# Kernel optimization log

Hardware: AMD Instinct MI355X
Metric: run time of the kernel (lower is better)

Reference implementation:

```python
import jax, jax.numpy as jnp
import numpy as np

K = 3  # kernel_size
STRIDE, PAD, DIL = 1, 1, 1


def conv2d(x, w, b):
    out = jax.lax.conv_general_dilated(
        x, w, (STRIDE, STRIDE), [(PAD, PAD), (PAD, PAD)],
        rhs_dilation=(DIL, DIL), dimension_numbers=('NCHW', 'OIHW', 'NCHW'))
    return out + b[None, :, None, None]


def bilinear_sample(x, sy, sx):
    """grid_sample(mode=bilinear, padding_mode=zeros, align_corners=True).
    x: (B,C,H,W); sy,sx: (B,K2,Ho,Wo) pixel coords. Returns (B,C,K2,Ho,Wo)."""
    B, C, H, W = x.shape
    y0 = jnp.floor(sy); x0 = jnp.floor(sx)
    y1 = y0 + 1.0;      x1 = x0 + 1.0
    wy1 = sy - y0; wy0 = 1.0 - wy1
    wx1 = sx - x0; wx0 = 1.0 - wx1
    x_flat = x.reshape(B, C, H * W)

    def gather(iy, ix):
        mask = ((iy >= 0) & (iy <= H - 1) & (ix >= 0) & (ix <= W - 1)).astype(x.dtype)
        iyc = jnp.clip(iy, 0, H - 1).astype(jnp.int32)
        ixc = jnp.clip(ix, 0, W - 1).astype(jnp.int32)
        idx = (iyc * W + ixc).reshape(B, 1, -1)
        v = jnp.take_along_axis(x_flat, idx, axis=2).reshape(B, C, *iy.shape[1:])
        return v * mask[:, None]

    return (gather(y0, x0) * (wy0 * wx0)[:, None]
            + gather(y0, x1) * (wy0 * wx1)[:, None]
            + gather(y1, x0) * (wy1 * wx0)[:, None]
            + gather(y1, x1) * (wy1 * wx1)[:, None])


def setup_inputs() -> dict:
    key = jax.random.key(0)
    ks = jax.random.split(key, 6)
    B, C, H, W = 4, 64, 128, 128
    O = 64
    x = jax.random.normal(ks[0], (B, C, H, W), jnp.float32)
    weight = jax.random.normal(ks[1], (O, C, K, K), jnp.float32) * (1.0 / (C * K * K) ** 0.5)
    bias = jax.random.normal(ks[2], (O,), jnp.float32) * 0.1
    offset_w = jax.random.normal(ks[3], (2 * K * K, C, K, K), jnp.float32) * 0.1 / (C * K * K) ** 0.5
    offset_b = jnp.zeros((2 * K * K,), jnp.float32)
    mod_w = jax.random.normal(ks[4], (K * K, C, K, K), jnp.float32) * (1.0 / (C * K * K) ** 0.5)
    mod_b = jnp.ones((K * K,), jnp.float32)
    return {"x": x, "weight": weight, "bias": bias,
            "offset_w": offset_w, "offset_b": offset_b,
            "mod_w": mod_w, "mod_b": mod_b}


def reference(x, weight, bias, offset_w, offset_b, mod_w, mod_b):
    B, C, H, W = x.shape
    O = weight.shape[0]
    K2 = K * K
    Ho = (H + 2 * PAD - DIL * (K - 1) - 1) // STRIDE + 1
    Wo = (W + 2 * PAD - DIL * (K - 1) - 1) // STRIDE + 1

    offsets = conv2d(x, offset_w, offset_b)                # (B, 2*K2, Ho, Wo)
    modul = jax.nn.sigmoid(conv2d(x, mod_w, mod_b))        # (B, K2, Ho, Wo)

    off = offsets.reshape(B, 2, K2, Ho, Wo)
    off_y, off_x = off[:, 0], off[:, 1]

    base_y, base_x = jnp.meshgrid(jnp.arange(Ho, dtype=jnp.float32),
                                  jnp.arange(Wo, dtype=jnp.float32), indexing='ij')
    base_y = base_y * STRIDE - PAD + (K // 2) * DIL
    base_x = base_x * STRIDE - PAD + (K // 2) * DIL
    koffs = jnp.arange(-(K // 2), K // 2 + 1, dtype=jnp.float32)
    ky, kx = jnp.meshgrid(koffs, koffs, indexing='ij')
    ky = ky.reshape(-1); kx = kx.reshape(-1)               # (K2,)

    sample_y = base_y[None, None] + ky[None, :, None, None] + off_y  # (B,K2,Ho,Wo)
    sample_x = base_x[None, None] + kx[None, :, None, None] + off_x
    # torch code normalizes to [-1,1] with align_corners=True; pixel coords are
    # recovered identically, so we sample directly at (sample_y, sample_x).

    sampled = bilinear_sample(x, sample_y, sample_x)       # (B,C,K2,Ho,Wo)

    w_flat = weight.reshape(O, C, K2)
    out = jnp.einsum('bckhw,ock->bohw', sampled, w_flat)   # groups=1

    mod_mean = jnp.mean(modul, axis=1, keepdims=True)      # (B,1,Ho,Wo)
    out = out * mod_mean + bias[None, :, None, None]
    return out
```

## Files before the change

### kernel.cpp

```cpp
#include <hip/hip_runtime.h>
#include <math.h>

#define K 3
#define K2 9
#define BB 4
#define C 64
#define H 128
#define W 128
#define O 64
#define HW (H*W)
#define Ho 128
#define Wo 128
#define TILE 64
#define TSTR 80

typedef _Float16 half4v __attribute__((ext_vector_type(4)));
typedef _Float16 half8v __attribute__((ext_vector_type(8)));
typedef float float4v __attribute__((ext_vector_type(4)));

__device__ __forceinline__ half8v bcast8(_Float16 w) {
    half8v v = {w, w, w, w, w, w, w, w};
    return v;
}

__global__ __launch_bounds__(256) void prep_all(
    const float* __restrict__ x,
    const float* __restrict__ weight,
    const float* __restrict__ offset_w,
    const float* __restrict__ mod_w,
    _Float16* __restrict__ xh,
    _Float16* __restrict__ wB,
    _Float16* __restrict__ wAB)
{
    int t = threadIdx.x;
    if (blockIdx.x < BB * H) {
        __shared__ _Float16 tile[W][68];
        int by = blockIdx.x;
        int y = by % H, b = by / H;
        int xq = t & 31, cr = t >> 5;
        #pragma unroll
        for (int g = 0; g < 8; g++) {
            int c = g * 8 + cr;
            float4v v = *(const float4v*)&x[(((size_t)b * C + c) * H + y) * W + xq * 4];
            tile[xq * 4 + 0][c] = (_Float16)v[0];
            tile[xq * 4 + 1][c] = (_Float16)v[1];
            tile[xq * 4 + 2][c] = (_Float16)v[2];
            tile[xq * 4 + 3][c] = (_Float16)v[3];
        }
        __syncthreads();
        int xp2 = t >> 1, hf = t & 1;
        const _Float16* src = &tile[xp2][hf * 32];
        _Float16* dst = xh + (((size_t)b * H + y) * W + xp2) * 64 + hf * 32;
        #pragma unroll
        for (int i = 0; i < 8; i++)
            *(half4v*)(dst + i * 4) = *(const half4v*)(src + i * 4);
    } else {
        int i = (blockIdx.x - BB * H) * 256 + t;
        if (i < K2 * 2 * 4 * 64 * 8) {
            int jj = i & 7;
            int lane = (i >> 3) & 63;
            int q4 = (i >> 9) & 3;
            int i2 = i >> 11;
            int tap = i2 >> 1, s = i2 & 1;
            int ch = s * 32 + ((lane >> 4) & 3) * 8 + jj;
            int o = q4 * 16 + (lane & 15);
            wB[i] = (_Float16)weight[(o * C + ch) * 9 + tap];
        }
        if (i < K2 * 2 * 2 * 64 * 8) {
            int jj = i & 7;
            int lane = (i >> 3) & 63;
            int jt = (i >> 9) & 1;
            int i2 = i >> 10;
            int tap = i2 >> 1, s = i2 & 1;
            int ch = s * 32 + ((lane >> 4) & 3) * 8 + jj;
            int n = jt * 16 + (lane & 15);
            float wv = 0.f;
            if (n < 27)
                wv = (n < 18) ? offset_w[(n * C + ch) * 9 + tap]
                              : mod_w[((n - 18) * C + ch) * 9 + tap];
            wAB[i] = (_Float16)wv;
        }
    }
}

__global__ __launch_bounds__(256) void fused_kernel(
    const _Float16* __restrict__ xh,
    const _Float16* __restrict__ wB,
    const _Float16* __restrict__ wAB,
    const float* __restrict__ bias,
    const float* __restrict__ offset_b,
    const float* __restrict__ mod_b,
    float* __restrict__ out)
{
    __shared__ _Float16 s_T[2][TILE][TSTR];
    __shared__ unsigned int s_ai[K2 * TILE];
    __shared__ half4v s_wgt[K2 * TILE];
    __shared__ float s_mm[TILE];
    float* s_res = (float*)&s_T[0][0][0];
    float* s_out = (float*)&s_T[0][0][0];

    int blk = blockIdx.x;
    int xcd = blk & 7, idx = blk >> 3;
    int b  = xcd >> 1;
    int h  = ((xcd & 1) << 6) | (idx >> 1);
    int wt = idx & 1;
    int t  = threadIdx.x;
    int q  = t >> 6;
    int lane = t & 63;
    int m16 = lane & 15;
    int quad = (lane >> 4) & 3;
    int w0 = wt * TILE;
    int px = lane;
    int gpx0 = q * 16 + (lane >> 3);
    int seg  = lane & 7;

    const _Float16* xb = xh + (size_t)b * HW * 64;

    float4v acc2[2];
    #pragma unroll
    for (int jt = 0; jt < 2; jt++) { float4v z = {0.f,0.f,0.f,0.f}; acc2[jt] = z; }

    #pragma unroll
    for (int pg = 0; pg < 2; pg++) {
        int ppx = gpx0 + pg * 8;
        int y = h - 1;
        int xv = w0 + ppx - 1;
        float m = ((y >= 0) ? 1.f : 0.f) * ((xv >= 0) ? 1.f : 0.f);
        int yc = max(y, 0), xc = max(xv, 0);
        const _Float16* src = xb + ((size_t)(yc * W + xc)) * 64 + seg * 8;
        half8v v = *(const half8v*)src;
        *(half8v*)&s_T[0][ppx][seg * 8] = v * bcast8((_Float16)m);
    }
    __syncthreads();

    #pragma unroll 1
    for (int tap = 0; tap < K2; tap++) {
        half8v pv[2]; _Float16 pm[2];
        if (tap < 8) {
            int tp = tap + 1;
            int ki = tp / 3, kj = tp % 3;
            int y = h + ki - 1;
            float my = (y >= 0 && y < H) ? 1.f : 0.f;
            int yc = min(max(y, 0), H - 1);
            #pragma unroll
            for (int pg = 0; pg < 2; pg++) {
                int ppx = gpx0 + pg * 8;
                int xv = w0 + ppx + kj - 1;
                pm[pg] = (_Float16)(my * ((xv >= 0 && xv < W) ? 1.f : 0.f));
                int xc = min(max(xv, 0), W - 1);
                pv[pg] = *(const half8v*)(xb + ((size_t)(yc * W + xc)) * 64 + seg * 8);
            }
        }
        int row = q * 16 + m16;
        #pragma unroll
        for (int s = 0; s < 2; s++) {
            half8v af = *(const half8v*)&s_T[tap & 1][row][s * 32 + quad * 8];
            #pragma unroll
            for (int jt = 0; jt < 2; jt++) {
                int widx = (((tap * 2 + s) * 2 + jt) * 64 + lane) * 8;
                half8v bf = *(const half8v*)(wAB + widx);
                acc2[jt] = __builtin_amdgcn_mfma_f32_16x16x32_f16(af, bf, acc2[jt], 0, 0, 0);
            }
        }
        if (tap < 8) {
            #pragma unroll
            for (int pg = 0; pg < 2; pg++)
                *(half8v*)&s_T[(tap + 1) & 1][gpx0 + pg * 8][seg * 8] = pv[pg] * bcast8(pm[pg]);
        }
        __syncthreads();
    }

    #pragma unroll
    for (int jt = 0; jt < 2; jt++) {
        int n = jt * 16 + m16;
        if (n < 27) {
            #pragma unroll
            for (int r = 0; r < 4; r++)
                s_res[n * 65 + q * 16 + quad * 4 + r] = acc2[jt][r];
        }
    }
    __syncthreads();

    #pragma unroll
    for (int ee = 0; ee < 3; ee++) {
        int e = t + ee * 256;
        if (e < K2 * TILE) {
            int k = e >> 6, p = e & 63;
            float offy = s_res[k * 65 + p] + offset_b[k];
            float offx = s_res[(9 + k) * 65 + p] + offset_b[9 + k];
            float sy = (float)(h + k / 3 - 1) + offy;
            float sx = (float)(w0 + p + k % 3 - 1) + offx;
            float fy = floorf(sy), fx = floorf(sx);
            int y0 = (int)fy, x0 = (int)fx;
            float wy1 = sy - fy, wx1 = sx - fx;
            int y0c = min(max(y0, 0), H - 1), y1c = min(max(y0 + 1, 0), H - 1);
            int x0c = min(max(x0, 0), W - 1), x1c = min(max(x0 + 1, 0), W - 1);
            s_ai[e] = (unsigned int)(y0c * W + x0c)
                    | ((unsigned int)(x1c - x0c) << 14)
                    | ((unsigned int)(y1c - y0c) << 15);
            float wg0 = (1.f - wy1) * ((y0 >= 0 && y0 < H) ? 1.f : 0.f);
            float wg1 = wy1 * ((y0 + 1 >= 0 && y0 + 1 < H) ? 1.f : 0.f);
            float wg2 = (1.f - wx1) * ((x0 >= 0 && x0 < W) ? 1.f : 0.f);
            float wg3 = wx1 * ((x0 + 1 >= 0 && x0 + 1 < W) ? 1.f : 0.f);
            half4v wp4;
            wp4[0] = (_Float16)(wg0 * wg2);
            wp4[1] = (_Float16)(wg0 * wg3);
            wp4[2] = (_Float16)(wg1 * wg2);
            wp4[3] = (_Float16)(wg1 * wg3);
            s_wgt[e] = wp4;
        }
    }
    if (t < TILE) {
        float sm = 0.f;
        #pragma unroll
        for (int m = 0; m < 9; m++) {
            float z = s_res[(18 + m) * 65 + t] + mod_b[m];
            sm += 1.f / (1.f + expf(-z));
        }
        s_mm[t] = sm * (1.f / 9.f);
    }
    __syncthreads();

    float4v acc[4];
    #pragma unroll
    for (int i = 0; i < 4; i++) { float4v z = {0.f,0.f,0.f,0.f}; acc[i] = z; }

    #pragma unroll
    for (int pg = 0; pg < 2; pg++) {
        int ppx = gpx0 + pg * 8;
        unsigned int ai = s_ai[ppx];
        half4v wg = s_wgt[ppx];
        int a00 = ai & 0x3FFF;
        int dxo = ((ai >> 14) & 1) * 64;
        int dyo = ((ai >> 15) & 1) * (W * 64);
        const _Float16* base = xb + (size_t)a00 * 64 + seg * 8;
        half8v r00 = *(const half8v*)(base);
        half8v r01 = *(const half8v*)(base + dxo);
        half8v r10 = *(const half8v*)(base + dyo);
        half8v r11 = *(const half8v*)(base + dyo + dxo);
        half8v v = r00 * bcast8(wg[0]) + r01 * bcast8(wg[1])
                 + r10 * bcast8(wg[2]) + r11 * bcast8(wg[3]);
        *(half8v*)&s_T[0][ppx][seg * 8] = v;
    }
    __syncthreads();

    #pragma unroll 1
    for (int tap = 0; tap < K2; tap++) {
        half8v rr[2][4]; half4v wgp[2];
        if (tap < 8) {
            #pragma unroll
            for (int pg = 0; pg < 2; pg++) {
                int e = (tap + 1) * 64 + gpx0 + pg * 8;
                unsigned int ai = s_ai[e];
                wgp[pg] = s_wgt[e];
                int a00 = ai & 0x3FFF;
                int dxo = ((ai >> 14) & 1) * 64;
                int dyo = ((ai >> 15) & 1) * (W * 64);
                const _Float16* base = xb + (size_t)a00 * 64 + seg * 8;
                rr[pg][0] = *(const half8v*)(base);
                rr[pg][1] = *(const half8v*)(base + dxo);
                rr[pg][2] = *(const half8v*)(base + dyo);
                rr[pg][3] = *(const half8v*)(base + dyo + dxo);
            }
        }
        #pragma unroll
        for (int s = 0; s < 2; s++) {
            int widx = (((tap * 2 + s) * 4 + q) * 64 + lane) * 8;
            half8v bf = *(const half8v*)(wB + widx);
            #pragma unroll
            for (int i = 0; i < 4; i++) {
                half8v af = *(const half8v*)&s_T[tap & 1][i * 16 + m16][s * 32 + quad * 8];
                acc[i] = __builtin_amdgcn_mfma_f32_16x16x32_f16(af, bf, acc[i], 0, 0, 0);
            }
        }
        if (tap < 8) {
            #pragma unroll
            for (int pg = 0; pg < 2; pg++) {
                half4v wg = wgp[pg];
                half8v v = rr[pg][0] * bcast8(wg[0]) + rr[pg][1] * bcast8(wg[1])
                         + rr[pg][2] * bcast8(wg[2]) + rr[pg][3] * bcast8(wg[3]);
                *(half8v*)&s_T[(tap + 1) & 1][gpx0 + pg * 8][seg * 8] = v;
            }
        }
        __syncthreads();
    }

    #pragma unroll
    for (int i = 0; i < 4; i++) {
        int o = q * 16 + m16;
        #pragma unroll
        for (int r = 0; r < 4; r++)
            s_out[o * 65 + i * 16 + quad * 4 + r] = acc[i][r];
    }
    __syncthreads();
    {
        float mm = s_mm[px];
        #pragma unroll
        for (int jj = 0; jj < 16; jj++) {
            int o = q * 16 + jj;
            out[(((size_t)b * O + o) * Ho + h) * Wo + w0 + px] =
                s_out[o * 65 + px] * mm + bias[o];
        }
    }
}

extern "C" void kernel_launch(void* const* d_in, const int* in_sizes, int n_in,
                              void* d_out, int out_size, void* d_ws, size_t ws_size,
                              hipStream_t stream) {
    const float* x        = (const float*)d_in[0];
    const float* weight   = (const float*)d_in[1];
    const float* bias     = (const float*)d_in[2];
    const float* offset_w = (const float*)d_in[3];
    const float* offset_b = (const float*)d_in[4];
    const float* mod_w    = (const float*)d_in[5];
    const float* mod_b    = (const float*)d_in[6];
    float* out = (float*)d_out;

    _Float16* wB  = (_Float16*)d_ws;
    _Float16* wAB = wB + 36864;
    _Float16* xh  = wAB + 18432;

    prep_all<<<BB * H + 144, 256, 0, stream>>>(
        x, weight, offset_w, mod_w, xh, wB, wAB);

    int nblk = BB * Ho * (Wo / TILE);
    fused_kernel<<<nblk, 256, 0, stream>>>(
        xh, wB, wAB, bias, offset_b, mod_b, out);
}
```

Baseline: 109.4 us.

## Give each wave a private LDS pixel tile to drop per-tap block barriers

Splits the shared double-buffered tile so each wave owns its own 16 pixels. Each wave stages, for all 64 channels, the pixels it then feeds to MFMA, which removes the __syncthreads inside both tap loops. In the main conv, each wave now computes all 64 output channels for its 16 pixels instead of 16 channels for all 64 pixels. That means four weight fragments are loaded from global per k-step instead of one. The exchange is fewer block barriers against more global weight traffic and more registers. Intra-wave LDS ordering now depends only on wave-level execution.

```diff
diff --git a/kernel.cpp b/kernel.cpp
--- a/kernel.cpp
+++ b/kernel.cpp
@@ -92,12 +92,12 @@
     const float* __restrict__ mod_b,
     float* __restrict__ out)
 {
-    __shared__ _Float16 s_T[2][TILE][TSTR];
+    __shared__ _Float16 s_W[4][2][16][TSTR];
     __shared__ unsigned int s_ai[K2 * TILE];
     __shared__ half4v s_wgt[K2 * TILE];
     __shared__ float s_mm[TILE];
-    float* s_res = (float*)&s_T[0][0][0];
-    float* s_out = (float*)&s_T[0][0][0];
+    float* s_res = (float*)&s_W[0][0][0][0];
+    float* s_out = (float*)&s_W[0][0][0][0];
 
     int blk = blockIdx.x;
     int xcd = blk & 7, idx = blk >> 3;
@@ -111,8 +111,8 @@
     int quad = (lane >> 4) & 3;
     int w0 = wt * TILE;
     int px = lane;
-    int gpx0 = q * 16 + (lane >> 3);
-    int seg  = lane & 7;
+    int p4 = lane >> 2;
+    int sg = lane & 3;
 
     const _Float16* xb = xh + (size_t)b * HW * 64;
 
@@ -120,41 +120,35 @@
     #pragma unroll
     for (int jt = 0; jt < 2; jt++) { float4v z = {0.f,0.f,0.f,0.f}; acc2[jt] = z; }
 
-    #pragma unroll
-    for (int pg = 0; pg < 2; pg++) {
-        int ppx = gpx0 + pg * 8;
+    {
         int y = h - 1;
-        int xv = w0 + ppx - 1;
+        int xv = w0 + q * 16 + p4 - 1;
         float m = ((y >= 0) ? 1.f : 0.f) * ((xv >= 0) ? 1.f : 0.f);
         int yc = max(y, 0), xc = max(xv, 0);
-        const _Float16* src = xb + ((size_t)(yc * W + xc)) * 64 + seg * 8;
-        half8v v = *(const half8v*)src;
-        *(half8v*)&s_T[0][ppx][seg * 8] = v * bcast8((_Float16)m);
-    }
-    __syncthreads();
+        const _Float16* src = xb + ((size_t)(yc * W + xc)) * 64 + sg * 8;
+        half8v vm = bcast8((_Float16)m);
+        *(half8v*)&s_W[q][0][p4][sg * 8]      = *(const half8v*)src * vm;
+        *(half8v*)&s_W[q][0][p4][32 + sg * 8] = *(const half8v*)(src + 32) * vm;
+    }
 
     #pragma unroll 1
     for (int tap = 0; tap < K2; tap++) {
-        half8v pv[2]; _Float16 pm[2];
+        half8v n0, n1; _Float16 nm;
         if (tap < 8) {
             int tp = tap + 1;
             int ki = tp / 3, kj = tp % 3;
             int y = h + ki - 1;
-            float my = (y >= 0 && y < H) ? 1.f : 0.f;
-            int yc = min(max(y, 0), H - 1);
-            #pragma unroll
-            for (int pg = 0; pg < 2; pg++) {
-                int ppx = gpx0 + pg * 8;
-                int xv = w0 + ppx + kj - 1;
-                pm[pg] = (_Float16)(my * ((xv >= 0 && xv < W) ? 1.f : 0.f));
-                int xc = min(max(xv, 0), W - 1);
-                pv[pg] = *(const half8v*)(xb + ((size_t)(yc * W + xc)) * 64 + seg * 8);
-            }
-        }
-        int row = q * 16 + m16;
+            int xv = w0 + q * 16 + p4 + kj - 1;
+            nm = (_Float16)(((y >= 0 && y < H) ? 1.f : 0.f) *
+                            ((xv >= 0 && xv < W) ? 1.f : 0.f));
+            int yc = min(max(y, 0), H - 1), xc = min(max(xv, 0), W - 1);
+            const _Float16* src = xb + ((size_t)(yc * W + xc)) * 64 + sg * 8;
+            n0 = *(const half8v*)src;
+            n1 = *(const half8v*)(src + 32);
+        }
         #pragma unroll
         for (int s = 0; s < 2; s++) {
-            half8v af = *(const half8v*)&s_T[tap & 1][row][s * 32 + quad * 8];
+            half8v af = *(const half8v*)&s_W[q][tap & 1][m16][s * 32 + quad * 8];
             #pragma unroll
             for (int jt = 0; jt < 2; jt++) {
                 int widx = (((tap * 2 + s) * 2 + jt) * 64 + lane) * 8;
@@ -163,13 +157,13 @@
             }
         }
         if (tap < 8) {
-            #pragma unroll
-            for (int pg = 0; pg < 2; pg++)
-                *(half8v*)&s_T[(tap + 1) & 1][gpx0 + pg * 8][seg * 8] = pv[pg] * bcast8(pm[pg]);
-        }
-        __syncthreads();
-    }
-
+            half8v vm = bcast8(nm);
+            *(half8v*)&s_W[q][(tap + 1) & 1][p4][sg * 8]      = n0 * vm;
+            *(half8v*)&s_W[q][(tap + 1) & 1][p4][32 + sg * 8] = n1 * vm;
+        }
+    }
+
+    __syncthreads();
     #pragma unroll
     for (int jt = 0; jt < 2; jt++) {
         int n = jt * 16 + m16;
@@ -225,72 +219,72 @@
     #pragma unroll
     for (int i = 0; i < 4; i++) { float4v z = {0.f,0.f,0.f,0.f}; acc[i] = z; }
 
-    #pragma unroll
-    for (int pg = 0; pg < 2; pg++) {
-        int ppx = gpx0 + pg * 8;
-        unsigned int ai = s_ai[ppx];
-        half4v wg = s_wgt[ppx];
+    {
+        int e = q * 16 + p4;
+        unsigned int ai = s_ai[e];
+        half4v wg = s_wgt[e];
         int a00 = ai & 0x3FFF;
         int dxo = ((ai >> 14) & 1) * 64;
         int dyo = ((ai >> 15) & 1) * (W * 64);
-        const _Float16* base = xb + (size_t)a00 * 64 + seg * 8;
-        half8v r00 = *(const half8v*)(base);
-        half8v r01 = *(const half8v*)(base + dxo);
-        half8v r10 = *(const half8v*)(base + dyo);
-        half8v r11 = *(const half8v*)(base + dyo + dxo);
-        half8v v = r00 * bcast8(wg[0]) + r01 * bcast8(wg[1])
-                 + r10 * bcast8(wg[2]) + r11 * bcast8(wg[3]);
-        *(half8v*)&s_T[0][ppx][seg * 8] = v;
-    }
-    __syncthreads();
+        const _Float16* base = xb + (size_t)a00 * 64 + sg * 8;
+        half8v v0 = *(const half8v*)(base)             * bcast8(wg[0])
+                  + *(const half8v*)(base + dxo)       * bcast8(wg[1])
+                  + *(const half8v*)(base + dyo)       * bcast8(wg[2])
+                  + *(const half8v*)(base + dyo + dxo) * bcast8(wg[3]);
+        half8v v1 = *(const half8v*)(base + 32)             * bcast8(wg[0])
+                  + *(const half8v*)(base + 32 + dxo)       * bcast8(wg[1])
+                  + *(const half8v*)(base + 32 + dyo)       * bcast8(wg[2])
+                  + *(const half8v*)(base + 32 + dyo + dxo) * bcast8(wg[3]);
+        *(half8v*)&s_W[q][0][p4][sg * 8]      = v0;
+        *(half8v*)&s_W[q][0][p4][32 + sg * 8] = v1;
+    }
 
     #pragma unroll 1
     for (int tap = 0; tap < K2; tap++) {
-        half8v rr[2][4]; half4v wgp[2];
+        half8v rr[8]; half4v wgp;
         if (tap < 8) {
+            int e = (tap + 1) * 64 + q * 16 + p4;
+            unsigned int ai = s_ai[e];
+            wgp = s_wgt[e];
+            int a00 = ai & 0x3FFF;
+            int dxo = ((ai >> 14) & 1) * 64;
+            int dyo = ((ai >> 15) & 1) * (W * 64);
+            const _Float16* base = xb + (size_t)a00 * 64 + sg * 8;
+            rr[0] = *(const half8v*)(base);
+            rr[1] = *(const half8v*)(base + dxo);
+            rr[2] = *(const half8v*)(base + dyo);
+            rr[3] = *(const half8v*)(base + dyo + dxo);
+            rr[4] = *(const half8v*)(base + 32);
+            rr[5] = *(const half8v*)(base + 32 + dxo);
+            rr[6] = *(const half8v*)(base + 32 + dyo);
+            rr[7] = *(const half8v*)(base + 32 + dyo + dxo);
+        }
+        #pragma unroll
+        for (int s = 0; s < 2; s++) {
+            half8v af = *(const half8v*)&s_W[q][tap & 1][m16][s * 32 + quad * 8];
             #pragma unroll
-            for (int pg = 0; pg < 2; pg++) {
-                int e = (tap + 1) * 64 + gpx0 + pg * 8;
-                unsigned int ai = s_ai[e];
-                wgp[pg] = s_wgt[e];
-                int a00 = ai & 0x3FFF;
-                int dxo = ((ai >> 14) & 1) * 64;
-                int dyo = ((ai >> 15) & 1) * (W * 64);
-                const _Float16* base = xb + (size_t)a00 * 64 + seg * 8;
-                rr[pg][0] = *(const half8v*)(base);
-                rr[pg][1] = *(const half8v*)(base + dxo);
-                rr[pg][2] = *(const half8v*)(base + dyo);
-                rr[pg][3] = *(const half8v*)(base + dyo + dxo);
+            for (int ot = 0; ot < 4; ot++) {
+                int widx = (((tap * 2 + s) * 4 + ot) * 64 + lane) * 8;
+                half8v bf = *(const half8v*)(wB + widx);
+                acc[ot] = __builtin_amdgcn_mfma_f32_16x16x32_f16(af, bf, acc[ot], 0, 0, 0);
             }
         }
-        #pragma unroll
-        for (int s = 0; s < 2; s++) {
-            int widx = (((tap * 2 + s) * 4 + q) * 64 + lane) * 8;
-            half8v bf = *(const half8v*)(wB + widx);
-            #pragma unroll
-            for (int i = 0; i < 4; i++) {
-                half8v af = *(const half8v*)&s_T[tap & 1][i * 16 + m16][s * 32 + quad * 8];
-                acc[i] = __builtin_amdgcn_mfma_f32_16x16x32_f16(af, bf, acc[i], 0, 0, 0);
-            }
-        }
         if (tap < 8) {
-            #pragma unroll
-            for (int pg = 0; pg < 2; pg++) {
-                half4v wg = wgp[pg];
-                half8v v = rr[pg][0] * bcast8(wg[0]) + rr[pg][1] * bcast8(wg[1])
-                         + rr[pg][2] * bcast8(wg[2]) + rr[pg][3] * bcast8(wg[3]);
-                *(half8v*)&s_T[(tap + 1) & 1][gpx0 + pg * 8][seg * 8] = v;
-            }
-        }
-        __syncthreads();
-    }
-
-    #pragma unroll
-    for (int i = 0; i < 4; i++) {
-        int o = q * 16 + m16;
+            half8v v0 = rr[0] * bcast8(wgp[0]) + rr[1] * bcast8(wgp[1])
+                      + rr[2] * bcast8(wgp[2]) + rr[3] * bcast8(wgp[3]);
+            half8v v1 = rr[4] * bcast8(wgp[0]) + rr[5] * bcast8(wgp[1])
+                      + rr[6] * bcast8(wgp[2]) + rr[7] * bcast8(wgp[3]);
+            *(half8v*)&s_W[q][(tap + 1) & 1][p4][sg * 8]      = v0;
+            *(half8v*)&s_W[q][(tap + 1) & 1][p4][32 + sg * 8] = v1;
+        }
+    }
+
+    __syncthreads();
+    #pragma unroll
+    for (int ot = 0; ot < 4; ot++) {
         #pragma unroll
         for (int r = 0; r < 4; r++)
-            s_out[o * 65 + i * 16 + quad * 4 + r] = acc[i][r];
+            s_out[(ot * 16 + m16) * 65 + q * 16 + quad * 4 + r] = acc[ot][r];
     }
     __syncthreads();
     {
```

New measurement: 114.0 us. 4.2% more time.

## Load offset-conv input fragments directly from global, drop LDS staging and barriers

Applied to the files above, without the earlier changes.

The offset/modulation conv stage no longer stages each tap's input row through a double-buffered LDS tile with a barrier per tap. Each lane now loads its MFMA operand straight from global (L2-cached NHWC fp16) and swaps the A/B roles so pixels sit on the B side, which changes how results are written to s_res. The loop is also unrolled by 3. This removes nine __syncthreads and the LDS round trips, at the cost of more uncoalesced global loads and exposed load latency.

```diff
diff --git a/kernel.cpp b/kernel.cpp
--- a/kernel.cpp
+++ b/kernel.cpp
@@ -111,6 +111,8 @@
     int quad = (lane >> 4) & 3;
     int w0 = wt * TILE;
     int px = lane;
+    int pxg = q * 16 + m16;
+    int chq = quad * 8;
     int gpx0 = q * 16 + (lane >> 3);
     int seg  = lane & 7;
 
@@ -120,63 +122,32 @@
     #pragma unroll
     for (int jt = 0; jt < 2; jt++) { float4v z = {0.f,0.f,0.f,0.f}; acc2[jt] = z; }
 
-    #pragma unroll
-    for (int pg = 0; pg < 2; pg++) {
-        int ppx = gpx0 + pg * 8;
-        int y = h - 1;
-        int xv = w0 + ppx - 1;
-        float m = ((y >= 0) ? 1.f : 0.f) * ((xv >= 0) ? 1.f : 0.f);
-        int yc = max(y, 0), xc = max(xv, 0);
-        const _Float16* src = xb + ((size_t)(yc * W + xc)) * 64 + seg * 8;
-        half8v v = *(const half8v*)src;
-        *(half8v*)&s_T[0][ppx][seg * 8] = v * bcast8((_Float16)m);
-    }
-    __syncthreads();
-
-    #pragma unroll 1
+    #pragma unroll 3
     for (int tap = 0; tap < K2; tap++) {
-        half8v pv[2]; _Float16 pm[2];
-        if (tap < 8) {
-            int tp = tap + 1;
-            int ki = tp / 3, kj = tp % 3;
-            int y = h + ki - 1;
-            float my = (y >= 0 && y < H) ? 1.f : 0.f;
-            int yc = min(max(y, 0), H - 1);
-            #pragma unroll
-            for (int pg = 0; pg < 2; pg++) {
-                int ppx = gpx0 + pg * 8;
-                int xv = w0 + ppx + kj - 1;
-                pm[pg] = (_Float16)(my * ((xv >= 0 && xv < W) ? 1.f : 0.f));
-                int xc = min(max(xv, 0), W - 1);
-                pv[pg] = *(const half8v*)(xb + ((size_t)(yc * W + xc)) * 64 + seg * 8);
-            }
-        }
-        int row = q * 16 + m16;
-        #pragma unroll
-        for (int s = 0; s < 2; s++) {
-            half8v af = *(const half8v*)&s_T[tap & 1][row][s * 32 + quad * 8];
-            #pragma unroll
-            for (int jt = 0; jt < 2; jt++) {
-                int widx = (((tap * 2 + s) * 2 + jt) * 64 + lane) * 8;
-                half8v bf = *(const half8v*)(wAB + widx);
-                acc2[jt] = __builtin_amdgcn_mfma_f32_16x16x32_f16(af, bf, acc2[jt], 0, 0, 0);
-            }
-        }
-        if (tap < 8) {
-            #pragma unroll
-            for (int pg = 0; pg < 2; pg++)
-                *(half8v*)&s_T[(tap + 1) & 1][gpx0 + pg * 8][seg * 8] = pv[pg] * bcast8(pm[pg]);
-        }
-        __syncthreads();
-    }
-
+        int ki = tap / 3, kj = tap % 3;
+        int y = h + ki - 1;
+        int xv = w0 + pxg + kj - 1;
+        _Float16 m = (_Float16)(((y >= 0 && y < H) ? 1.f : 0.f) *
+                                ((xv >= 0 && xv < W) ? 1.f : 0.f));
+        int yc = min(max(y, 0), H - 1), xc = min(max(xv, 0), W - 1);
+        const _Float16* src = xb + ((size_t)(yc * W + xc)) * 64 + chq;
+        half8v vm = bcast8(m);
+        half8v b0 = *(const half8v*)src * vm;
+        half8v b1 = *(const half8v*)(src + 32) * vm;
+        #pragma unroll
+        for (int jt = 0; jt < 2; jt++) {
+            half8v a0 = *(const half8v*)(wAB + (((tap * 2 + 0) * 2 + jt) * 64 + lane) * 8);
+            half8v a1 = *(const half8v*)(wAB + (((tap * 2 + 1) * 2 + jt) * 64 + lane) * 8);
+            acc2[jt] = __builtin_amdgcn_mfma_f32_16x16x32_f16(a0, b0, acc2[jt], 0, 0, 0);
+            acc2[jt] = __builtin_amdgcn_mfma_f32_16x16x32_f16(a1, b1, acc2[jt], 0, 0, 0);
+        }
+    }
     #pragma unroll
     for (int jt = 0; jt < 2; jt++) {
-        int n = jt * 16 + m16;
-        if (n < 27) {
-            #pragma unroll
-            for (int r = 0; r < 4; r++)
-                s_res[n * 65 + q * 16 + quad * 4 + r] = acc2[jt][r];
+        #pragma unroll
+        for (int r = 0; r < 4; r++) {
+            int n = jt * 16 + quad * 4 + r;
+            if (n < 27) s_res[n * 65 + pxg] = acc2[jt][r];
         }
     }
     __syncthreads();
```

After: 112.5 us. 2.9% more time.
